# Optimization experiments

Hardware: AMD Instinct MI355X
Metric: run time of the kernel (lower is better)

## Reference

```python
import jax, jax.numpy as jnp
import numpy as np

B, S, D, H, NH = 4, 4096, 256, 1024, 8


def _layernorm(x, g, b, eps=1e-5):
    mu = jnp.mean(x, axis=-1, keepdims=True)
    var = jnp.var(x, axis=-1, keepdims=True)
    return (x - mu) / jnp.sqrt(var + eps) * g + b


def setup_inputs() -> dict:
    key = jax.random.key(0)
    ks = jax.random.split(key, 3)
    std = 0.02
    return {
        "x": jax.random.normal(ks[0], (B, S, D), dtype=jnp.float32),
        "gamma1": jnp.ones((D,), jnp.float32),
        "beta1": jnp.zeros((D,), jnp.float32),
        "W1": jax.random.normal(ks[1], (D, H), dtype=jnp.float32) * std,
        "b1": jnp.zeros((H,), jnp.float32),
        "W2": jax.random.normal(ks[2], (H, D), dtype=jnp.float32) * std,
        "b2": jnp.zeros((D,), jnp.float32),
        "gamma2": jnp.ones((D,), jnp.float32),
        "beta2": jnp.zeros((D,), jnp.float32),
        "n_head": NH,
    }


def reference(x, gamma1, beta1, W1, b1, W2, b2, gamma2, beta2, n_head):
    # First-call path of CachedLocalMultiheadAttention: single-head softmax
    # attention on raw x, scale = (d_model // n_head) ** -0.5, no masks.
    scale = (x.shape[-1] // n_head) ** -0.5
    scores = jnp.einsum('bqd,bkd->bqk', x, x) * scale  # [B,S,S]
    attn = jax.nn.softmax(scores, axis=-1)
    a = jnp.einsum('bqk,bkd->bqd', attn, x)
    # residual + LayerNorm (dropouts are identity in eval)
    h = _layernorm(a + x, gamma1, beta1)
    # positionwise FFN
    f = jnp.maximum(h @ W1 + b1, 0.0) @ W2 + b2
    return _layernorm(f + h, gamma2, beta2)
```

## Files before the change

kernel.cpp:

```cpp
#include <hip/hip_runtime.h>


#define DIM 256
#define SEQ 4096
#define BATCHN 4
#define HID 1024
#define NROW (BATCHN * SEQ)

typedef __attribute__((ext_vector_type(8))) short short8;
typedef __attribute__((ext_vector_type(4))) float float4v;
typedef __attribute__((ext_vector_type(16))) float float16v;

static __device__ __forceinline__ unsigned int f2bf1(float f) {
  unsigned int b = __float_as_uint(f);
  return (b + 0x7fffu + ((b >> 16) & 1u)) >> 16;
}
static __device__ __forceinline__ unsigned int pack2bf(float lo, float hi) {
  return f2bf1(lo) | (f2bf1(hi) << 16);
}
static __device__ __forceinline__ float bf2f(unsigned short v) {
  return __uint_as_float(((unsigned int)v) << 16);
}
static __device__ __forceinline__ float bflo(unsigned int p) { return __uint_as_float(p << 16); }
static __device__ __forceinline__ float bfhi(unsigned int p) { return __uint_as_float(p & 0xffff0000u); }

static __device__ __forceinline__ void bar_lgkm() {
  __asm__ __volatile__("s_waitcnt lgkmcnt(0)" ::: "memory");
  __builtin_amdgcn_s_barrier();
  __asm__ __volatile__("" ::: "memory");
}

static __device__ __forceinline__ void pl32swap(unsigned int& a, unsigned int& b) {
  __asm__ __volatile__("v_permlane32_swap_b32 %0, %1" : "+v"(a), "+v"(b));
}

union FragU { uint4 u; short8 s; };

__global__ __launch_bounds__(256, 2) void attn_part(
    const float* __restrict__ x,
    unsigned short* __restrict__ P01, unsigned short* __restrict__ P23,
    float* __restrict__ lpart) {
  __shared__ unsigned short Krow[32][264];
  __shared__ unsigned short Vt[256][40];

  const int tid = threadIdx.x;
  const int l = tid & 63;
  const int n = l & 31;
  const int half = l >> 5;
  const int b = blockIdx.y;
  const int z = blockIdx.z;
  const int qw = (blockIdx.x << 7) + ((tid >> 6) << 5);
  const float* xb = x + (size_t)b * SEQ * DIM;
  const float scale = 0.17677669529663687f;
  const float SHIFT = 46.0f;

  short8 qf[16];
#pragma unroll
  for (int c = 0; c < 16; c++) {
    const float* qp = xb + (size_t)(qw + n) * DIM + (c << 4) + (half << 3);
    float4 a0 = *reinterpret_cast<const float4*>(qp);
    float4 a1 = *reinterpret_cast<const float4*>(qp + 4);
    short8 q8;
    q8[0] = (short)f2bf1(a0.x); q8[1] = (short)f2bf1(a0.y);
    q8[2] = (short)f2bf1(a0.z); q8[3] = (short)f2bf1(a0.w);
    q8[4] = (short)f2bf1(a1.x); q8[5] = (short)f2bf1(a1.y);
    q8[6] = (short)f2bf1(a1.z); q8[7] = (short)f2bf1(a1.w);
    qf[c] = q8;
  }

  float16v o[8];
#pragma unroll
  for (int nb = 0; nb < 8; nb++)
#pragma unroll
    for (int r = 0; r < 16; r++) o[nb][r] = 0.f;
  float lsum = 0.f;

  const int kp = tid & 15;
  const int sd2 = (tid >> 4) << 4;
  const int kbase = z << 10;

  float4 e0[4];
  {
    const float* sp = xb + (size_t)(kbase + (kp << 1)) * DIM + sd2;
#pragma unroll
    for (int j = 0; j < 4; j++) e0[j] = *reinterpret_cast<const float4*>(sp + (j << 2));
  }

  for (int k0 = kbase; k0 < kbase + 1024; k0 += 32) {
    float4 e1[4];
    {
      const float* sp = xb + (size_t)(k0 + (kp << 1) + 1) * DIM + sd2;
#pragma unroll
      for (int j = 0; j < 4; j++) e1[j] = *reinterpret_cast<const float4*>(sp + (j << 2));
    }

    bar_lgkm();
#pragma unroll
    for (int j = 0; j < 4; j++) {
      *reinterpret_cast<uint2*>(&Krow[(kp << 1) + 0][sd2 + (j << 2)]) =
          make_uint2(pack2bf(e0[j].x, e0[j].y), pack2bf(e0[j].z, e0[j].w));
      *reinterpret_cast<uint2*>(&Krow[(kp << 1) + 1][sd2 + (j << 2)]) =
          make_uint2(pack2bf(e1[j].x, e1[j].y), pack2bf(e1[j].z, e1[j].w));
    }
#pragma unroll
    for (int j = 0; j < 4; j++) {
      const int d = sd2 + (j << 2);
      *reinterpret_cast<unsigned int*>(&Vt[d + 0][kp << 1]) = pack2bf(e0[j].x, e1[j].x);
      *reinterpret_cast<unsigned int*>(&Vt[d + 1][kp << 1]) = pack2bf(e0[j].y, e1[j].y);
      *reinterpret_cast<unsigned int*>(&Vt[d + 2][kp << 1]) = pack2bf(e0[j].z, e1[j].z);
      *reinterpret_cast<unsigned int*>(&Vt[d + 3][kp << 1]) = pack2bf(e0[j].w, e1[j].w);
    }
    bar_lgkm();

    {
      const int kn = (k0 + 32 < kbase + 1024) ? (k0 + 32) : k0;
      const float* spn = xb + (size_t)(kn + (kp << 1)) * DIM + sd2;
#pragma unroll
      for (int j = 0; j < 4; j++) e0[j] = *reinterpret_cast<const float4*>(spn + (j << 2));
    }

    float16v s;
#pragma unroll
    for (int r = 0; r < 16; r++) s[r] = 0.f;
#pragma unroll
    for (int c = 0; c < 16; c++) {
      short8 a = *reinterpret_cast<const short8*>(&Krow[n][(c << 4) + (half << 3)]);
      s = __builtin_amdgcn_mfma_f32_32x32x16_bf16(a, qf[c], s, 0, 0, 0);
    }
    float p[16];
#pragma unroll
    for (int r = 0; r < 16; r++) {
      p[r] = __expf(fmaf(s[r], scale, -SHIFT));
      lsum += p[r];
    }
    unsigned int Pr[8];
#pragma unroll
    for (int g = 0; g < 4; g++) {
      Pr[2 * g + 0] = pack2bf(p[4 * g + 0], p[4 * g + 1]);
      Pr[2 * g + 1] = pack2bf(p[4 * g + 2], p[4 * g + 3]);
    }
    pl32swap(Pr[0], Pr[2]); pl32swap(Pr[1], Pr[3]);
    pl32swap(Pr[4], Pr[6]); pl32swap(Pr[5], Pr[7]);
    FragU f0, f1;
    f0.u = make_uint4(Pr[0], Pr[1], Pr[2], Pr[3]);
    f1.u = make_uint4(Pr[4], Pr[5], Pr[6], Pr[7]);

#pragma unroll
    for (int kk = 0; kk < 2; kk++) {
      const short8 pf = kk ? f1.s : f0.s;
#pragma unroll
      for (int nb = 0; nb < 8; nb++) {
        short8 vf = *reinterpret_cast<const short8*>(&Vt[(nb << 5) + n][(kk << 4) + (half << 3)]);
        o[nb] = __builtin_amdgcn_mfma_f32_32x32x16_bf16(pf, vf, o[nb], 0, 0, 0);
      }
    }
  }

  lsum += __shfl_xor(lsum, 32);
  if (l < 32) lpart[(z << 14) + (b << 12) + qw + l] = lsum;

  unsigned short* Op = ((z < 2) ? P01 : P23) + ((size_t)(z & 1) << 22);
#pragma unroll
  for (int nb = 0; nb < 8; nb++) {
#pragma unroll
    for (int r = 0; r < 16; r++) {
      const int q = (r & 3) + ((r >> 2) << 3) + (half << 2);
      Op[((size_t)(b << 12) + qw + q) * DIM + (nb << 5) + n] = (unsigned short)f2bf1(o[nb][r]);
    }
  }
}

__global__ __launch_bounds__(256) void merge_prep(
    const unsigned short* __restrict__ P01, const unsigned short* __restrict__ P23,
    const float* __restrict__ lpart, const float* __restrict__ x,
    const float* __restrict__ g1, const float* __restrict__ be1,
    unsigned short* __restrict__ hbf,
    const float* __restrict__ W1, const float* __restrict__ W2,
    unsigned short* __restrict__ W1Tb, unsigned short* __restrict__ W2Tb) {
  __shared__ float Ls[64][65];
  const int tid = threadIdx.x;
  if (blockIdx.x >= 512) {
    const int bid = blockIdx.x - 512;
    const bool second = bid >= 64;
    const int wid = bid - (second ? 64 : 0);
    const int N = second ? DIM : HID;
    const float* src = second ? W2 : W1;
    unsigned short* dst = second ? W2Tb : W1Tb;
    const int ntn = N >> 6;
    const int k0 = (wid / ntn) << 6, n0 = (wid % ntn) << 6;

    const int r = tid >> 2, cg = (tid & 3) << 4;
#pragma unroll
    for (int q = 0; q < 4; q++) {
      float4 v = *reinterpret_cast<const float4*>(src + (size_t)(k0 + r) * N + n0 + cg + (q << 2));
      Ls[r][cg + (q << 2) + 0] = v.x; Ls[r][cg + (q << 2) + 1] = v.y;
      Ls[r][cg + (q << 2) + 2] = v.z; Ls[r][cg + (q << 2) + 3] = v.w;
    }
    __syncthreads();
    const int j = tid >> 2, part = tid & 3;
    const int kbl = part >> 1, ko = (part & 1) << 4, kl = part << 4;
    unsigned int pk[8];
#pragma unroll
    for (int q = 0; q < 8; q++) pk[q] = pack2bf(Ls[kl + 2 * q][j], Ls[kl + 2 * q + 1][j]);
    unsigned short* dp = dst + (((size_t)((k0 >> 5) + kbl) * N + n0 + j) << 5) + ko;
    *reinterpret_cast<uint4*>(dp) = make_uint4(pk[0], pk[1], pk[2], pk[3]);
    *reinterpret_cast<uint4*>(dp + 8) = make_uint4(pk[4], pk[5], pk[6], pk[7]);
    return;
  }
  const int row = (blockIdx.x << 5) + (tid >> 3);
  const int c0 = (tid & 7) << 5;
  const float rl = 1.0f / (lpart[row] + lpart[NROW + row] +
                           lpart[2 * NROW + row] + lpart[3 * NROW + row]);
  const float* px = x + (size_t)row * DIM + c0;

  float v[32];
#pragma unroll
  for (int j = 0; j < 32; j++) v[j] = 0.f;
#pragma unroll
  for (int part = 0; part < 4; part++) {
    const unsigned short* pb = ((part < 2) ? P01 : P23) + ((size_t)(part & 1) << 22) +
                               (size_t)row * DIM + c0;
#pragma unroll
    for (int j = 0; j < 8; j++) {
      uint2 raw = *reinterpret_cast<const uint2*>(pb + (j << 2));
      v[(j << 2) + 0] += bflo(raw.x); v[(j << 2) + 1] += bfhi(raw.x);
      v[(j << 2) + 2] += bflo(raw.y); v[(j << 2) + 3] += bfhi(raw.y);
    }
  }
#pragma unroll
  for (int j = 0; j < 8; j++) {
    float4 xr = *reinterpret_cast<const float4*>(px + (j << 2));
    v[(j << 2) + 0] = fmaf(v[(j << 2) + 0], rl, xr.x);
    v[(j << 2) + 1] = fmaf(v[(j << 2) + 1], rl, xr.y);
    v[(j << 2) + 2] = fmaf(v[(j << 2) + 2], rl, xr.z);
    v[(j << 2) + 3] = fmaf(v[(j << 2) + 3], rl, xr.w);
  }
  float s = 0.f, s2 = 0.f;
#pragma unroll
  for (int j = 0; j < 32; j++) { s += v[j]; s2 = fmaf(v[j], v[j], s2); }
  s += __shfl_xor(s, 1); s += __shfl_xor(s, 2); s += __shfl_xor(s, 4);
  s2 += __shfl_xor(s2, 1); s2 += __shfl_xor(s2, 2); s2 += __shfl_xor(s2, 4);
  const float mean = s * (1.f / 256.f);
  const float var = s2 * (1.f / 256.f) - mean * mean;
  const float rstd = rsqrtf(var + 1e-5f);
  unsigned short* hb = hbf + (size_t)row * DIM + c0;
  unsigned int pk[16];
#pragma unroll
  for (int j = 0; j < 8; j++) {
    float4 gv = *reinterpret_cast<const float4*>(g1 + c0 + (j << 2));
    float4 bv = *reinterpret_cast<const float4*>(be1 + c0 + (j << 2));
    float o0 = fmaf((v[(j << 2) + 0] - mean) * rstd, gv.x, bv.x);
    float o1 = fmaf((v[(j << 2) + 1] - mean) * rstd, gv.y, bv.y);
    float o2 = fmaf((v[(j << 2) + 2] - mean) * rstd, gv.z, bv.z);
    float o3 = fmaf((v[(j << 2) + 3] - mean) * rstd, gv.w, bv.w);
    pk[2 * j] = pack2bf(o0, o1); pk[2 * j + 1] = pack2bf(o2, o3);
  }
#pragma unroll
  for (int q = 0; q < 4; q++)
    *reinterpret_cast<uint4*>(hb + (q << 3)) =
        make_uint4(pk[4 * q], pk[4 * q + 1], pk[4 * q + 2], pk[4 * q + 3]);
}

__global__ __launch_bounds__(256) void ffn1_mfma(
    const unsigned short* __restrict__ hbf, const unsigned short* __restrict__ W1Tb,
    const float* __restrict__ b1, unsigned short* __restrict__ ub) {
  __shared__ unsigned short As[128][264];
  __shared__ unsigned short Bs[128][40];
  const int tid = threadIdx.x;
  const int w = tid >> 6;
  const int l = tid & 63;
  const int tx = l & 15;
  const int p = l >> 4;
  const int wm = w >> 1, wn = w & 1;
  const int r0 = blockIdx.x << 7, c0 = blockIdx.y << 7;

  float4v acc[4][4];
#pragma unroll
  for (int i = 0; i < 4; i++)
#pragma unroll
    for (int j = 0; j < 4; j++) acc[i][j] = (float4v){0.f, 0.f, 0.f, 0.f};

  {
    const unsigned short* base = hbf + (size_t)r0 * DIM;
#pragma unroll
    for (int j = 0; j < 16; j++) {
      const int fo = (tid << 3) + (j << 11);
      uint4 v = *reinterpret_cast<const uint4*>(base + fo);
      *reinterpret_cast<uint4*>(&As[fo >> 8][fo & 255]) = v;
    }
  }
  for (int kb = 0; kb < 8; kb++) {
    __syncthreads();
    {
      const unsigned short* base = W1Tb + (((size_t)kb * HID + c0) << 5);
#pragma unroll
      for (int j = 0; j < 2; j++) {
        const int fo = (tid << 3) + (j << 11);
        uint4 v = *reinterpret_cast<const uint4*>(base + fo);
        *reinterpret_cast<uint4*>(&Bs[fo >> 5][fo & 31]) = v;
      }
    }
    __syncthreads();
    short8 af[4], bf[4];
#pragma unroll
    for (int f = 0; f < 4; f++) {
      af[f] = *reinterpret_cast<const short8*>(&As[(wm << 6) + (f << 4) + tx][(kb << 5) + (p << 3)]);
      bf[f] = *reinterpret_cast<const short8*>(&Bs[(wn << 6) + (f << 4) + tx][p << 3]);
    }
#pragma unroll
    for (int i = 0; i < 4; i++)
#pragma unroll
      for (int j = 0; j < 4; j++)
        acc[i][j] = __builtin_amdgcn_mfma_f32_16x16x32_bf16(af[i], bf[j], acc[i][j], 0, 0, 0);
  }
  float bias[4];
#pragma unroll
  for (int j = 0; j < 4; j++) bias[j] = b1[c0 + (wn << 6) + (j << 4) + tx];
  __syncthreads();
  unsigned short (*Ep)[72] = reinterpret_cast<unsigned short(*)[72]>(&As[0][0] + w * 2304);
#pragma unroll
  for (int hh = 0; hh < 2; hh++) {
#pragma unroll
    for (int i2 = 0; i2 < 2; i2++) {
      const int i = (hh << 1) + i2;
#pragma unroll
      for (int j = 0; j < 4; j++)
#pragma unroll
        for (int rg = 0; rg < 4; rg++)
          Ep[(i2 << 4) + (p << 2) + rg][(j << 4) + tx] =
              (unsigned short)f2bf1(fmaxf(acc[i][j][rg] + bias[j], 0.f));
    }
    __syncthreads();
    const int cb = l >> 5, r32 = l & 31;
    const int grow = r0 + (wm << 6) + (hh << 5) + r32;
    const int kb = (c0 >> 5) + (wn << 1) + cb;
    unsigned short* up = ub + (((size_t)kb * NROW + grow) << 5);
#pragma unroll
    for (int q = 0; q < 4; q++)
      *reinterpret_cast<uint4*>(up + (q << 3)) =
          *reinterpret_cast<const uint4*>(&Ep[r32][(cb << 5) + (q << 3)]);
    __syncthreads();
  }
}

__global__ __launch_bounds__(256) void ffn2_mfma(
    const unsigned short* __restrict__ ub, const unsigned short* __restrict__ W2Tb,
    const float* __restrict__ b2, const unsigned short* __restrict__ hbf,
    const float* __restrict__ g2, const float* __restrict__ be2,
    float* __restrict__ out) {
  __shared__ unsigned short As[32][72];
  __shared__ unsigned short Bs[256][72];
  __shared__ float2 red[32][4];
  const int tid = threadIdx.x;
  const int w = tid >> 6;
  const int l = tid & 63;
  const int tx = l & 15;
  const int p = l >> 4;
  const int r0 = blockIdx.x << 5;

  float4v acc[2][4];
#pragma unroll
  for (int i = 0; i < 2; i++)
#pragma unroll
    for (int j = 0; j < 4; j++) acc[i][j] = (float4v){0.f, 0.f, 0.f, 0.f};

  for (int kb = 0; kb < 16; kb++) {
    __syncthreads();
    {
      const int flat = tid << 3;
      const int kbl = flat >> 10;
      const int rem = flat & 1023;
      const int row = rem >> 5, off = rem & 31;
      uint4 v = *reinterpret_cast<const uint4*>(
          ub + ((((size_t)(2 * kb + kbl)) * NROW + r0 + row) << 5) + off);
      *reinterpret_cast<uint4*>(&As[row][(kbl << 5) + off]) = v;
    }
    {
#pragma unroll
      for (int j = 0; j < 8; j++) {
        const int flat = (tid << 3) + (j << 11);
        const int kbl = flat >> 13;
        const int rem = flat & 8191;
        const int nn = rem >> 5, off = rem & 31;
        uint4 v = *reinterpret_cast<const uint4*>(
            W2Tb + ((((size_t)(2 * kb + kbl)) * DIM + nn) << 5) + off);
        *reinterpret_cast<uint4*>(&Bs[nn][(kbl << 5) + off]) = v;
      }
    }
    __syncthreads();
#pragma unroll
    for (int ks = 0; ks < 2; ks++) {
      short8 af[2], bf[4];
#pragma unroll
      for (int i = 0; i < 2; i++)
        af[i] = *reinterpret_cast<const short8*>(&As[(i << 4) + tx][(ks << 5) + (p << 3)]);
#pragma unroll
      for (int j = 0; j < 4; j++)
        bf[j] = *reinterpret_cast<const short8*>(&Bs[(w << 6) + (j << 4) + tx][(ks << 5) + (p << 3)]);
#pragma unroll
      for (int i = 0; i < 2; i++)
#pragma unroll
        for (int j = 0; j < 4; j++)
          acc[i][j] = __builtin_amdgcn_mfma_f32_16x16x32_bf16(af[i], bf[j], acc[i][j], 0, 0, 0);
    }
  }

  float bias[4];
#pragma unroll
  for (int j = 0; j < 4; j++) bias[j] = b2[(w << 6) + (j << 4) + tx];
#pragma unroll
  for (int i = 0; i < 2; i++)
#pragma unroll
    for (int rg = 0; rg < 4; rg++) {
      const int row = r0 + (i << 4) + (p << 2) + rg;
#pragma unroll
      for (int j = 0; j < 4; j++)
        acc[i][j][rg] += bias[j] + bf2f(hbf[(size_t)row * DIM + (w << 6) + (j << 4) + tx]);
    }
#pragma unroll
  for (int i = 0; i < 2; i++)
#pragma unroll
    for (int rg = 0; rg < 4; rg++) {
      float s = acc[i][0][rg] + acc[i][1][rg] + acc[i][2][rg] + acc[i][3][rg];
      float s2 = 0.f;
#pragma unroll
      for (int j = 0; j < 4; j++) s2 = fmaf(acc[i][j][rg], acc[i][j][rg], s2);
      s += __shfl_xor(s, 1); s += __shfl_xor(s, 2);
      s += __shfl_xor(s, 4); s += __shfl_xor(s, 8);
      s2 += __shfl_xor(s2, 1); s2 += __shfl_xor(s2, 2);
      s2 += __shfl_xor(s2, 4); s2 += __shfl_xor(s2, 8);
      if (tx == 0) red[(i << 4) + (p << 2) + rg][w] = make_float2(s, s2);
    }
  __syncthreads();
#pragma unroll
  for (int i = 0; i < 2; i++)
#pragma unroll
    for (int rg = 0; rg < 4; rg++) {
      const int rl = (i << 4) + (p << 2) + rg;
      float2 a0 = red[rl][0], a1 = red[rl][1], a2 = red[rl][2], a3 = red[rl][3];
      const float S = (a0.x + a1.x) + (a2.x + a3.x);
      const float S2 = (a0.y + a1.y) + (a2.y + a3.y);
      const float mean = S * (1.f / 256.f);
      const float var = S2 * (1.f / 256.f) - mean * mean;
      const float rstd = rsqrtf(var + 1e-5f);
      const int row = r0 + rl;
#pragma unroll
      for (int j = 0; j < 4; j++) {
        const int col = (w << 6) + (j << 4) + tx;
        out[(size_t)row * DIM + col] =
            fmaf((acc[i][j][rg] - mean) * rstd, g2[col], be2[col]);
      }
    }
}

extern "C" void kernel_launch(void* const* d_in, const int* in_sizes, int n_in,
                              void* d_out, int out_size, void* d_ws, size_t ws_size,
                              hipStream_t stream) {
  const float* x = (const float*)d_in[0];
  const float* g1 = (const float*)d_in[1];
  const float* be1 = (const float*)d_in[2];
  const float* W1 = (const float*)d_in[3];
  const float* b1 = (const float*)d_in[4];
  const float* W2 = (const float*)d_in[5];
  const float* b2 = (const float*)d_in[6];
  const float* g2 = (const float*)d_in[7];
  const float* be2 = (const float*)d_in[8];
  float* out = (float*)d_out;
  char* wsb = (char*)d_ws;

  unsigned short* P01 = (unsigned short*)d_out;
  unsigned short* P23 = (unsigned short*)wsb;
  float* lp = (float*)(wsb + ((size_t)16 << 20));
  unsigned short* u = (unsigned short*)wsb;
  unsigned short* hbf = (unsigned short*)(wsb + ((size_t)32 << 20));
  unsigned short* W2Tb = (unsigned short*)(wsb + ((size_t)40 << 20));
  unsigned short* W1Tb = (unsigned short*)(wsb + ((size_t)40 << 20) + ((size_t)512 << 10));

  attn_part<<<dim3(SEQ / 128, BATCHN, 4), 256, 0, stream>>>(x, P01, P23, lp);
  merge_prep<<<dim3(512 + 128), 256, 0, stream>>>(P01, P23, lp, x, g1, be1, hbf,
                                                  W1, W2, W1Tb, W2Tb);
  ffn1_mfma<<<dim3(NROW / 128, HID / 128), 256, 0, stream>>>(hbf, W1Tb, b1, u);
  ffn2_mfma<<<dim3(NROW / 32), 256, 0, stream>>>(u, W2Tb, b2, hbf, g2, be2, out);
}
```

Before: 235.8 us.

## Fuse split-K attention merge and LayerNorm into attention via last-block counter

Merges the separate merge/LayerNorm kernel into the attention kernel. The last of the four key-split blocks for each query tile, detected with an atomic counter, sums the partial outputs, adds the residual and applies LayerNorm. The weight transposes run in extra grid blocks of the same launch. This removes one kernel launch and its tail, at the cost of a memset, threadfences, an atomic and serialized merge work in the last-arriving block.

```diff
diff --git a/kernel.cpp b/kernel.cpp
--- a/kernel.cpp
+++ b/kernel.cpp
@@ -36,19 +36,55 @@
 
 union FragU { uint4 u; short8 s; };
 
-__global__ __launch_bounds__(256, 2) void attn_part(
+__global__ __launch_bounds__(256, 2) void attn_fused(
     const float* __restrict__ x,
     unsigned short* __restrict__ P01, unsigned short* __restrict__ P23,
-    float* __restrict__ lpart) {
+    float* __restrict__ lpart, int* __restrict__ cnt,
+    const float* __restrict__ g1, const float* __restrict__ be1,
+    unsigned short* __restrict__ hbf,
+    const float* __restrict__ W1, const float* __restrict__ W2,
+    unsigned short* __restrict__ W1Tb, unsigned short* __restrict__ W2Tb) {
   __shared__ unsigned short Krow[32][264];
   __shared__ unsigned short Vt[256][40];
+  __shared__ int s_old;
 
   const int tid = threadIdx.x;
+  const int b = blockIdx.y;
+  const int z = blockIdx.z;
+
+  if (blockIdx.x >= 32) {
+    float (*Ls)[65] = reinterpret_cast<float(*)[65]>(&Krow[0][0]);
+    const int wid = ((blockIdx.x - 32) << 4) + (b << 2) + z;
+    const bool second = wid >= 64;
+    const int pid = wid - (second ? 64 : 0);
+    const int N = second ? DIM : HID;
+    const float* src = second ? W2 : W1;
+    unsigned short* dst = second ? W2Tb : W1Tb;
+    const int ntn = N >> 6;
+    const int k0 = (pid / ntn) << 6, n0 = (pid % ntn) << 6;
+
+    const int r = tid >> 2, cg = (tid & 3) << 4;
+#pragma unroll
+    for (int q = 0; q < 4; q++) {
+      float4 v = *reinterpret_cast<const float4*>(src + (size_t)(k0 + r) * N + n0 + cg + (q << 2));
+      Ls[r][cg + (q << 2) + 0] = v.x; Ls[r][cg + (q << 2) + 1] = v.y;
+      Ls[r][cg + (q << 2) + 2] = v.z; Ls[r][cg + (q << 2) + 3] = v.w;
+    }
+    __syncthreads();
+    const int j = tid >> 2, part = tid & 3;
+    const int kbl = part >> 1, ko = (part & 1) << 4, kl = part << 4;
+    unsigned int pk[8];
+#pragma unroll
+    for (int q = 0; q < 8; q++) pk[q] = pack2bf(Ls[kl + 2 * q][j], Ls[kl + 2 * q + 1][j]);
+    unsigned short* dp = dst + (((size_t)((k0 >> 5) + kbl) * N + n0 + j) << 5) + ko;
+    *reinterpret_cast<uint4*>(dp) = make_uint4(pk[0], pk[1], pk[2], pk[3]);
+    *reinterpret_cast<uint4*>(dp + 8) = make_uint4(pk[4], pk[5], pk[6], pk[7]);
+    return;
+  }
+
   const int l = tid & 63;
   const int n = l & 31;
   const int half = l >> 5;
-  const int b = blockIdx.y;
-  const int z = blockIdx.z;
   const int qw = (blockIdx.x << 7) + ((tid >> 6) << 5);
   const float* xb = x + (size_t)b * SEQ * DIM;
   const float scale = 0.17677669529663687f;
@@ -168,97 +204,69 @@
       Op[((size_t)(b << 12) + qw + q) * DIM + (nb << 5) + n] = (unsigned short)f2bf1(o[nb][r]);
     }
   }
-}
-
-__global__ __launch_bounds__(256) void merge_prep(
-    const unsigned short* __restrict__ P01, const unsigned short* __restrict__ P23,
-    const float* __restrict__ lpart, const float* __restrict__ x,
-    const float* __restrict__ g1, const float* __restrict__ be1,
-    unsigned short* __restrict__ hbf,
-    const float* __restrict__ W1, const float* __restrict__ W2,
-    unsigned short* __restrict__ W1Tb, unsigned short* __restrict__ W2Tb) {
-  __shared__ float Ls[64][65];
-  const int tid = threadIdx.x;
-  if (blockIdx.x >= 512) {
-    const int bid = blockIdx.x - 512;
-    const bool second = bid >= 64;
-    const int wid = bid - (second ? 64 : 0);
-    const int N = second ? DIM : HID;
-    const float* src = second ? W2 : W1;
-    unsigned short* dst = second ? W2Tb : W1Tb;
-    const int ntn = N >> 6;
-    const int k0 = (wid / ntn) << 6, n0 = (wid % ntn) << 6;
-
-    const int r = tid >> 2, cg = (tid & 3) << 4;
-#pragma unroll
-    for (int q = 0; q < 4; q++) {
-      float4 v = *reinterpret_cast<const float4*>(src + (size_t)(k0 + r) * N + n0 + cg + (q << 2));
-      Ls[r][cg + (q << 2) + 0] = v.x; Ls[r][cg + (q << 2) + 1] = v.y;
-      Ls[r][cg + (q << 2) + 2] = v.z; Ls[r][cg + (q << 2) + 3] = v.w;
-    }
-    __syncthreads();
-    const int j = tid >> 2, part = tid & 3;
-    const int kbl = part >> 1, ko = (part & 1) << 4, kl = part << 4;
-    unsigned int pk[8];
-#pragma unroll
-    for (int q = 0; q < 8; q++) pk[q] = pack2bf(Ls[kl + 2 * q][j], Ls[kl + 2 * q + 1][j]);
-    unsigned short* dp = dst + (((size_t)((k0 >> 5) + kbl) * N + n0 + j) << 5) + ko;
-    *reinterpret_cast<uint4*>(dp) = make_uint4(pk[0], pk[1], pk[2], pk[3]);
-    *reinterpret_cast<uint4*>(dp + 8) = make_uint4(pk[4], pk[5], pk[6], pk[7]);
-    return;
-  }
-  const int row = (blockIdx.x << 5) + (tid >> 3);
+
+  __threadfence();
+  __syncthreads();
+  if (tid == 0) s_old = atomicAdd(&cnt[(b << 5) + blockIdx.x], 1);
+  __syncthreads();
+  if (s_old != 3) return;
+  __threadfence();
+
+  const int R0 = (b << 12) + (blockIdx.x << 7);
   const int c0 = (tid & 7) << 5;
-  const float rl = 1.0f / (lpart[row] + lpart[NROW + row] +
-                           lpart[2 * NROW + row] + lpart[3 * NROW + row]);
-  const float* px = x + (size_t)row * DIM + c0;
-
-  float v[32];
-#pragma unroll
-  for (int j = 0; j < 32; j++) v[j] = 0.f;
-#pragma unroll
-  for (int part = 0; part < 4; part++) {
-    const unsigned short* pb = ((part < 2) ? P01 : P23) + ((size_t)(part & 1) << 22) +
-                               (size_t)row * DIM + c0;
+#pragma unroll 1
+  for (int ch = 0; ch < 4; ch++) {
+    const int row = R0 + (ch << 5) + (tid >> 3);
+    const float rl = 1.0f / (lpart[row] + lpart[NROW + row] +
+                             lpart[2 * NROW + row] + lpart[3 * NROW + row]);
+    const float* px = x + (size_t)row * DIM + c0;
+    float v[32];
+#pragma unroll
+    for (int j = 0; j < 32; j++) v[j] = 0.f;
+#pragma unroll
+    for (int part = 0; part < 4; part++) {
+      const unsigned short* pb = ((part < 2) ? P01 : P23) + ((size_t)(part & 1) << 22) +
+                                 (size_t)row * DIM + c0;
+#pragma unroll
+      for (int j = 0; j < 8; j++) {
+        uint2 raw = *reinterpret_cast<const uint2*>(pb + (j << 2));
+        v[(j << 2) + 0] += bflo(raw.x); v[(j << 2) + 1] += bfhi(raw.x);
+        v[(j << 2) + 2] += bflo(raw.y); v[(j << 2) + 3] += bfhi(raw.y);
+      }
+    }
 #pragma unroll
     for (int j = 0; j < 8; j++) {
-      uint2 raw = *reinterpret_cast<const uint2*>(pb + (j << 2));
-      v[(j << 2) + 0] += bflo(raw.x); v[(j << 2) + 1] += bfhi(raw.x);
-      v[(j << 2) + 2] += bflo(raw.y); v[(j << 2) + 3] += bfhi(raw.y);
-    }
-  }
-#pragma unroll
-  for (int j = 0; j < 8; j++) {
-    float4 xr = *reinterpret_cast<const float4*>(px + (j << 2));
-    v[(j << 2) + 0] = fmaf(v[(j << 2) + 0], rl, xr.x);
-    v[(j << 2) + 1] = fmaf(v[(j << 2) + 1], rl, xr.y);
-    v[(j << 2) + 2] = fmaf(v[(j << 2) + 2], rl, xr.z);
-    v[(j << 2) + 3] = fmaf(v[(j << 2) + 3], rl, xr.w);
-  }
-  float s = 0.f, s2 = 0.f;
-#pragma unroll
-  for (int j = 0; j < 32; j++) { s += v[j]; s2 = fmaf(v[j], v[j], s2); }
-  s += __shfl_xor(s, 1); s += __shfl_xor(s, 2); s += __shfl_xor(s, 4);
-  s2 += __shfl_xor(s2, 1); s2 += __shfl_xor(s2, 2); s2 += __shfl_xor(s2, 4);
-  const float mean = s * (1.f / 256.f);
-  const float var = s2 * (1.f / 256.f) - mean * mean;
-  const float rstd = rsqrtf(var + 1e-5f);
-  unsigned short* hb = hbf + (size_t)row * DIM + c0;
-  unsigned int pk[16];
-#pragma unroll
-  for (int j = 0; j < 8; j++) {
-    float4 gv = *reinterpret_cast<const float4*>(g1 + c0 + (j << 2));
-    float4 bv = *reinterpret_cast<const float4*>(be1 + c0 + (j << 2));
-    float o0 = fmaf((v[(j << 2) + 0] - mean) * rstd, gv.x, bv.x);
-    float o1 = fmaf((v[(j << 2) + 1] - mean) * rstd, gv.y, bv.y);
-    float o2 = fmaf((v[(j << 2) + 2] - mean) * rstd, gv.z, bv.z);
-    float o3 = fmaf((v[(j << 2) + 3] - mean) * rstd, gv.w, bv.w);
-    pk[2 * j] = pack2bf(o0, o1); pk[2 * j + 1] = pack2bf(o2, o3);
-  }
-#pragma unroll
-  for (int q = 0; q < 4; q++)
-    *reinterpret_cast<uint4*>(hb + (q << 3)) =
-        make_uint4(pk[4 * q], pk[4 * q + 1], pk[4 * q + 2], pk[4 * q + 3]);
+      float4 xr = *reinterpret_cast<const float4*>(px + (j << 2));
+      v[(j << 2) + 0] = fmaf(v[(j << 2) + 0], rl, xr.x);
+      v[(j << 2) + 1] = fmaf(v[(j << 2) + 1], rl, xr.y);
+      v[(j << 2) + 2] = fmaf(v[(j << 2) + 2], rl, xr.z);
+      v[(j << 2) + 3] = fmaf(v[(j << 2) + 3], rl, xr.w);
+    }
+    float s = 0.f, s2 = 0.f;
+#pragma unroll
+    for (int j = 0; j < 32; j++) { s += v[j]; s2 = fmaf(v[j], v[j], s2); }
+    s += __shfl_xor(s, 1); s += __shfl_xor(s, 2); s += __shfl_xor(s, 4);
+    s2 += __shfl_xor(s2, 1); s2 += __shfl_xor(s2, 2); s2 += __shfl_xor(s2, 4);
+    const float mean = s * (1.f / 256.f);
+    const float var = s2 * (1.f / 256.f) - mean * mean;
+    const float rstd = rsqrtf(var + 1e-5f);
+    unsigned short* hb = hbf + (size_t)row * DIM + c0;
+    unsigned int pk[16];
+#pragma unroll
+    for (int j = 0; j < 8; j++) {
+      float4 gv = *reinterpret_cast<const float4*>(g1 + c0 + (j << 2));
+      float4 bv = *reinterpret_cast<const float4*>(be1 + c0 + (j << 2));
+      float o0 = fmaf((v[(j << 2) + 0] - mean) * rstd, gv.x, bv.x);
+      float o1 = fmaf((v[(j << 2) + 1] - mean) * rstd, gv.y, bv.y);
+      float o2 = fmaf((v[(j << 2) + 2] - mean) * rstd, gv.z, bv.z);
+      float o3 = fmaf((v[(j << 2) + 3] - mean) * rstd, gv.w, bv.w);
+      pk[2 * j] = pack2bf(o0, o1); pk[2 * j + 1] = pack2bf(o2, o3);
+    }
+#pragma unroll
+    for (int q = 0; q < 4; q++)
+      *reinterpret_cast<uint4*>(hb + (q << 3)) =
+          make_uint4(pk[4 * q], pk[4 * q + 1], pk[4 * q + 2], pk[4 * q + 3]);
+  }
 }
 
 __global__ __launch_bounds__(256) void ffn1_mfma(
@@ -471,14 +479,15 @@
   unsigned short* P01 = (unsigned short*)d_out;
   unsigned short* P23 = (unsigned short*)wsb;
   float* lp = (float*)(wsb + ((size_t)16 << 20));
+  int* cnt = (int*)(wsb + ((size_t)16 << 20) + ((size_t)256 << 10));
   unsigned short* u = (unsigned short*)wsb;
   unsigned short* hbf = (unsigned short*)(wsb + ((size_t)32 << 20));
   unsigned short* W2Tb = (unsigned short*)(wsb + ((size_t)40 << 20));
   unsigned short* W1Tb = (unsigned short*)(wsb + ((size_t)40 << 20) + ((size_t)512 << 10));
 
-  attn_part<<<dim3(SEQ / 128, BATCHN, 4), 256, 0, stream>>>(x, P01, P23, lp);
-  merge_prep<<<dim3(512 + 128), 256, 0, stream>>>(P01, P23, lp, x, g1, be1, hbf,
-                                                  W1, W2, W1Tb, W2Tb);
+  hipMemsetAsync(cnt, 0, 128 * sizeof(int), stream);
+  attn_fused<<<dim3(40, BATCHN, 4), 256, 0, stream>>>(
+      x, P01, P23, lp, cnt, g1, be1, hbf, W1, W2, W1Tb, W2Tb);
   ffn1_mfma<<<dim3(NROW / 128, HID / 128), 256, 0, stream>>>(hbf, W1Tb, b1, u);
   ffn2_mfma<<<dim3(NROW / 32), 256, 0, stream>>>(u, W2Tb, b2, hbf, g2, be2, out);
 }
```

Result: slower. 327.0 us (+38.7%).
